# Kernel tuning notes

Measured on AMD Instinct MI355X. Metric: run time of the kernel, lower is better.

## Reference

```python
import jax, jax.numpy as jnp
import numpy as np

ITERS = 10   # self.iters
REG = 0.1    # self.reg
EPS = 1e-12  # F.normalize eps


def setup_inputs() -> dict:
    key = jax.random.key(0)
    k1, k2 = jax.random.split(key)
    b, n_s, h = 64, 512, 1024
    x = jax.random.normal(k1, (b, n_s, h), dtype=jnp.float32)
    y = jax.random.normal(k2, (b, n_s, h), dtype=jnp.float32)
    return {"x": x, "y": y}


def _l2_normalize(t):
    n = jnp.sqrt(jnp.sum(t * t, axis=-1, keepdims=True))
    return t / jnp.maximum(n, EPS)


def reference(x, y):
    # CosineScorer.score(x, y, get_diag=False) with temperature=1
    xn = _l2_normalize(x)
    yn = _l2_normalize(y)
    scores = jnp.einsum('bmh,bnh->bmn', xn, yn)  # (b, n_s, n_s)
    b, m, n = scores.shape

    # uniform log marginals: -log(n_s)
    log_mu = jnp.full((b, m), -jnp.log(jnp.float32(m)), dtype=scores.dtype)
    log_nu = jnp.full((b, n), -jnp.log(jnp.float32(n)), dtype=scores.dtype)

    # log_ipot: iterative proximal point OT in log space
    A = scores / jnp.float32(REG)

    def step(carry, _):
        v, T = carry
        Q = A + T                                              # (b, m, n)
        u = log_mu - jax.nn.logsumexp(Q + v[:, None, :], axis=2)
        v_new = log_nu - jax.nn.logsumexp(Q + u[:, :, None], axis=1)
        T_new = Q + u[:, :, None] + v_new[:, None, :]
        return (v_new, T_new), None

    init = (log_nu, jnp.zeros_like(scores))
    (_, T), _ = jax.lax.scan(step, init, None, length=ITERS)

    matching = jnp.exp(T)
    return jnp.sum(scores * matching, axis=(1, 2))  # (b,)
```

## Files before the change

### kernel.cpp

```cpp
#include <hip/hip_runtime.h>
#include <hip/hip_fp16.h>

#define NB 64
#define NS 512
#define NH 1024
#define NITERS 10

#define LOG_INV_NS (-6.238324625039508f)

using half8 = _Float16 __attribute__((ext_vector_type(8)));
using f32x4 = float __attribute__((ext_vector_type(4)));

__global__ __launch_bounds__(512) void gemm_fused(
    const float* __restrict__ x, const float* __restrict__ y,
    _Float16* __restrict__ Sh) {
  __shared__ _Float16 As[2][256][72];
  __shared__ _Float16 Bs[2][256][72];
  __shared__ float invA[256], invB[256];

  int blk = blockIdx.x;
  int b = blk & 63;
  int tile = blk >> 6;
  int tm = (tile >> 1) * 256, tn = (tile & 1) * 256;
  int tid = threadIdx.x;
  int wid = tid >> 6, lane = tid & 63;
  int wr = (wid >> 2) * 128;
  int wc = (wid & 3) * 64;
  int fr = lane & 15, fq = lane >> 4;

  int srow = tid >> 1;
  int skh = (tid & 1) * 16;
  const float* xb = x + ((size_t)b * NS + tm + srow) * NH + skh;
  const float* yb = y + ((size_t)b * NS + tn + srow) * NH + skh;

  f32x4 acc[8][4] = {};
  float4 rx[4], ry[4];
  float sqx = 0.f, sqy = 0.f;

#define GLOAD(K0)                                                     \
  do {                                                                \
    const float4* px = (const float4*)(xb + (K0));                    \
    const float4* py = (const float4*)(yb + (K0));                    \
    rx[0] = px[0]; rx[1] = px[1]; rx[2] = px[2]; rx[3] = px[3];       \
    ry[0] = py[0]; ry[1] = py[1]; ry[2] = py[2]; ry[3] = py[3];       \
  } while (0)

#define CAST_WRITE(BUF, COL)                                          \
  do {                                                                \
    alignas(16) _Float16 ta[16];                                      \
    alignas(16) _Float16 tb[16];                                      \
    _Pragma("unroll") for (int j = 0; j < 4; ++j) {                   \
      float4 v = rx[j];                                               \
      ta[4 * j + 0] = (_Float16)v.x; ta[4 * j + 1] = (_Float16)v.y;   \
      ta[4 * j + 2] = (_Float16)v.z; ta[4 * j + 3] = (_Float16)v.w;   \
      sqx += v.x * v.x + v.y * v.y + v.z * v.z + v.w * v.w;           \
    }                                                                 \
    _Pragma("unroll") for (int j = 0; j < 4; ++j) {                   \
      float4 v = ry[j];                                               \
      tb[4 * j + 0] = (_Float16)v.x; tb[4 * j + 1] = (_Float16)v.y;   \
      tb[4 * j + 2] = (_Float16)v.z; tb[4 * j + 3] = (_Float16)v.w;   \
      sqy += v.x * v.x + v.y * v.y + v.z * v.z + v.w * v.w;           \
    }                                                                 \
    *(half8*)&As[BUF][srow][(COL) + skh + 0] = *(half8*)&ta[0];       \
    *(half8*)&As[BUF][srow][(COL) + skh + 8] = *(half8*)&ta[8];       \
    *(half8*)&Bs[BUF][srow][(COL) + skh + 0] = *(half8*)&tb[0];       \
    *(half8*)&Bs[BUF][srow][(COL) + skh + 8] = *(half8*)&tb[8];       \
  } while (0)

  GLOAD(0);
  CAST_WRITE(0, 0);
  GLOAD(32);
  CAST_WRITE(0, 32);
  GLOAD(64);
  asm volatile("s_waitcnt lgkmcnt(0)" ::: "memory");
  __builtin_amdgcn_sched_barrier(0);
  __builtin_amdgcn_s_barrier();
  __builtin_amdgcn_sched_barrier(0);

  for (int s = 0; s < 16; ++s) {
    int cur = s & 1;
    {
      half8 bf[4];
#pragma unroll
      for (int j = 0; j < 4; ++j)
        bf[j] = *(const half8*)&Bs[cur][wc + 16 * j + fr][8 * fq];
#pragma unroll
      for (int i = 0; i < 8; ++i) {
        half8 af = *(const half8*)&As[cur][wr + 16 * i + fr][8 * fq];
#pragma unroll
        for (int j = 0; j < 4; ++j)
          acc[i][j] = __builtin_amdgcn_mfma_f32_16x16x32_f16(af, bf[j], acc[i][j], 0, 0, 0);
      }
    }
    if (s < 15) {
      CAST_WRITE(cur ^ 1, 0);
      GLOAD((s + 1) * 64 + 32);
    }
    {
      half8 bf[4];
#pragma unroll
      for (int j = 0; j < 4; ++j)
        bf[j] = *(const half8*)&Bs[cur][wc + 16 * j + fr][32 + 8 * fq];
#pragma unroll
      for (int i = 0; i < 8; ++i) {
        half8 af = *(const half8*)&As[cur][wr + 16 * i + fr][32 + 8 * fq];
#pragma unroll
        for (int j = 0; j < 4; ++j)
          acc[i][j] = __builtin_amdgcn_mfma_f32_16x16x32_f16(af, bf[j], acc[i][j], 0, 0, 0);
      }
    }
    if (s < 15) {
      CAST_WRITE(cur ^ 1, 32);
      if (s < 14) GLOAD((s + 2) * 64);
    }
    asm volatile("s_waitcnt lgkmcnt(0)" ::: "memory");
    __builtin_amdgcn_sched_barrier(0);
    __builtin_amdgcn_s_barrier();
    __builtin_amdgcn_sched_barrier(0);
  }
#undef GLOAD
#undef CAST_WRITE

  sqx += __shfl_xor(sqx, 1, 64);
  sqy += __shfl_xor(sqy, 1, 64);
  if ((tid & 1) == 0) {
    invA[srow] = 1.0f / fmaxf(sqrtf(sqx), 1e-12f);
    invB[srow] = 1.0f / fmaxf(sqrtf(sqy), 1e-12f);
  }
  __syncthreads();

  _Float16* Sb = Sh + (size_t)b * NS * NS;
#pragma unroll
  for (int i = 0; i < 8; ++i)
#pragma unroll
    for (int j = 0; j < 4; ++j) {
      int rr = wr + 16 * i + 4 * fq;
      int cc = wc + 16 * j + fr;
      float ib = invB[cc];
#pragma unroll
      for (int p = 0; p < 4; ++p)
        Sb[(size_t)(tm + rr + p) * NS + tn + cc] =
            (_Float16)(acc[i][j][p] * invA[rr + p] * ib);
    }
}

__global__ __launch_bounds__(256) void u_kernel(
    const _Float16* __restrict__ Sh, const float* __restrict__ W,
    float* __restrict__ U, float f, int first) {
  __shared__ float Wt[8][65];
  int blk = blockIdx.x;
  int bs = blk & 7, rest = blk >> 3;
  int rowgrp = rest & 31, bq = rest >> 5;
  int b = bq * 8 + bs;
  int t = threadIdx.x;
  if (!first) {
#pragma unroll
    for (int i = 0; i < 2; ++i) {
      int idx = t + 256 * i;
      Wt[idx & 7][idx >> 3] = W[b * NS + idx];
    }
    __syncthreads();
  }
  int w = t >> 6, l = t & 63;
  float wn[8];
#pragma unroll
  for (int e = 0; e < 8; ++e) wn[e] = first ? LOG_INV_NS : Wt[e][l];
  int m0 = rowgrp * 16 + w * 4;
  const _Float16* Sb = Sh + ((size_t)b * NS + m0) * NS + 8 * l;
  float sum[4] = {0.f, 0.f, 0.f, 0.f};
#pragma unroll
  for (int k = 0; k < 4; ++k) {
    half8 hv = *(const half8*)(Sb + (size_t)k * NS);
#pragma unroll
    for (int e = 0; e < 8; ++e) sum[k] += __expf(fmaf(f, (float)hv[e], wn[e]));
  }
#pragma unroll
  for (int o = 32; o; o >>= 1) {
#pragma unroll
    for (int k = 0; k < 4; ++k) sum[k] += __shfl_xor(sum[k], o, 64);
  }
  if (l == 0) {
#pragma unroll
    for (int k = 0; k < 4; ++k)
      U[b * NS + m0 + k] = LOG_INV_NS - __logf(sum[k]);
  }
}

__global__ __launch_bounds__(256) void v_kernel(
    const _Float16* __restrict__ Sh, const float* __restrict__ U,
    float* __restrict__ V, float* __restrict__ W,
    float f, int first, int last, float* __restrict__ outPart) {
  __shared__ float Ul[NS];
  __shared__ float partC[64][33];
  __shared__ float partD[64][33];
  __shared__ float redC[4][33];
  __shared__ float redD[4][33];
  int blk = blockIdx.x;
  int b = blk & 63;
  int ng = blk >> 6;
  int t = threadIdx.x;
  Ul[t] = U[b * NS + t];
  Ul[t + 256] = U[b * NS + t + 256];
  __syncthreads();

  int oct = t & 3;
  int mc = t >> 2;
  const _Float16* Sb = Sh + (size_t)b * NS * NS + (size_t)(mc * 8) * NS + ng * 32 + oct * 8;
  float c[8] = {}, d[8] = {};
#pragma unroll
  for (int i = 0; i < 8; ++i) {
    half8 hv = *(const half8*)(Sb + (size_t)i * NS);
    float um = Ul[mc * 8 + i];
#pragma unroll
    for (int e = 0; e < 8; ++e) {
      float sv = (float)hv[e];
      float ev = __expf(fmaf(f, sv, um));
      c[e] += ev;
      d[e] = fmaf(sv, ev, d[e]);
    }
  }
#pragma unroll
  for (int e = 0; e < 8; ++e) {
    partC[mc][oct * 8 + e] = c[e];
    partD[mc][oct * 8 + e] = d[e];
  }
  __syncthreads();
  {
    int ci = t & 31, seg = t >> 5;
    float cc = 0.f, dd = 0.f;
#pragma unroll
    for (int k = 0; k < 8; ++k) {
      cc += partC[seg * 8 + k][ci];
      dd += partD[seg * 8 + k][ci];
    }
    cc += __shfl_xor(cc, 32, 64);
    dd += __shfl_xor(dd, 32, 64);
    int w = t >> 6, l = t & 63;
    if (l < 32) { redC[w][l] = cc; redD[w][l] = dd; }
  }
  __syncthreads();
  if (t < 32) {
    float cc = redC[0][t] + redC[1][t] + redC[2][t] + redC[3][t];
    float vnew = LOG_INV_NS - __logf(cc);
    int n = b * NS + ng * 32 + t;
    float vold = first ? 0.f : V[n];
    V[n] = vnew;
    W[n] = 2.f * vnew - vold;
    if (last) {
      float dd = redD[0][t] + redD[1][t] + redD[2][t] + redD[3][t];
      float r = dd / cc;
      r += __shfl_xor(r, 16, 64);
      r += __shfl_xor(r, 8, 64);
      r += __shfl_xor(r, 4, 64);
      r += __shfl_xor(r, 2, 64);
      r += __shfl_xor(r, 1, 64);
      if (t == 0) outPart[b * 16 + ng] = r * (1.0f / (float)NS);
    }
  }
}

__global__ void combine_kernel(const float* __restrict__ outPart, float* __restrict__ out) {
  int b = threadIdx.x;
  float s = 0.f;
#pragma unroll
  for (int k = 0; k < 16; ++k) s += outPart[b * 16 + k];
  out[b] = s;
}

extern "C" void kernel_launch(void* const* d_in, const int* in_sizes, int n_in,
                              void* d_out, int out_size, void* d_ws, size_t ws_size,
                              hipStream_t stream) {
  (void)in_sizes; (void)n_in; (void)out_size; (void)ws_size;
  const float* x = (const float*)d_in[0];
  const float* y = (const float*)d_in[1];
  float* out = (float*)d_out;

  char* ws = (char*)d_ws;
  _Float16* Sh = (_Float16*)ws;
  float* fregion = (float*)(ws + (size_t)NB * NS * NS * 2);
  float* U = fregion;
  float* V = U + NB * NS;
  float* W = V + NB * NS;
  float* outPart = W + NB * NS;

  gemm_fused<<<256, 512, 0, stream>>>(x, y, Sh);

  for (int t = 1; t <= NITERS; ++t) {
    float f = 10.0f * (float)t;
    u_kernel<<<2048, 256, 0, stream>>>(Sh, W, U, f, t == 1 ? 1 : 0);
    v_kernel<<<1024, 256, 0, stream>>>(Sh, U, V, W, f, t == 1 ? 1 : 0,
                                       t == NITERS ? 1 : 0, outPart);
  }
  combine_kernel<<<1, 64, 0, stream>>>(outPart, out);
}
```

Measured before the change: 192.8 us.

## Stage fp32 tiles via direct global-to-LDS loads with XOR swizzle

```diff
diff --git a/kernel.cpp b/kernel.cpp
--- a/kernel.cpp
+++ b/kernel.cpp
@@ -11,11 +11,16 @@
 using half8 = _Float16 __attribute__((ext_vector_type(8)));
 using f32x4 = float __attribute__((ext_vector_type(4)));
 
+#define GLOAD_LDS(G, L)                                                  \
+  __builtin_amdgcn_global_load_lds(                                      \
+      (const __attribute__((address_space(1))) unsigned int*)(G),        \
+      (__attribute__((address_space(3))) unsigned int*)(L), 16, 0, 0)
+
 __global__ __launch_bounds__(512) void gemm_fused(
     const float* __restrict__ x, const float* __restrict__ y,
     _Float16* __restrict__ Sh) {
-  __shared__ _Float16 As[2][256][72];
-  __shared__ _Float16 Bs[2][256][72];
+  __shared__ float As32[2][8192];
+  __shared__ float Bs32[2][8192];
   __shared__ float invA[256], invB[256];
 
   int blk = blockIdx.x;
@@ -28,104 +33,103 @@
   int wc = (wid & 3) * 64;
   int fr = lane & 15, fq = lane >> 4;
 
-  int srow = tid >> 1;
-  int skh = (tid & 1) * 16;
-  const float* xb = x + ((size_t)b * NS + tm + srow) * NH + skh;
-  const float* yb = y + ((size_t)b * NS + tn + srow) * NH + skh;
+  int rql = wid * 32 + (lane >> 3);
+  int colf = 4 * ((lane & 7) ^ (rql & 7));
+  const float* xg0 = x + ((size_t)(b * NS + tm + rql)) * NH + colf;
+  const float* yg0 = y + ((size_t)(b * NS + tn + rql)) * NH + colf;
 
   f32x4 acc[8][4] = {};
-  float4 rx[4], ry[4];
-  float sqx = 0.f, sqy = 0.f;
-
-#define GLOAD(K0)                                                     \
-  do {                                                                \
-    const float4* px = (const float4*)(xb + (K0));                    \
-    const float4* py = (const float4*)(yb + (K0));                    \
-    rx[0] = px[0]; rx[1] = px[1]; rx[2] = px[2]; rx[3] = px[3];       \
-    ry[0] = py[0]; ry[1] = py[1]; ry[2] = py[2]; ry[3] = py[3];       \
+  float pa[4] = {0.f, 0.f, 0.f, 0.f};
+  float pb[4] = {0.f, 0.f, 0.f, 0.f};
+
+#define GSTAGE(CH, BUF)                                                  \
+  do {                                                                   \
+    int k0g = (CH) * 32;                                                 \
+    _Pragma("unroll") for (int q = 0; q < 4; ++q) {                      \
+      GLOAD_LDS(xg0 + (size_t)(q * 8) * NH + k0g,                        \
+                &As32[BUF][wid * 1024 + q * 256]);                       \
+      GLOAD_LDS(yg0 + (size_t)(q * 8) * NH + k0g,                        \
+                &Bs32[BUF][wid * 1024 + q * 256]);                       \
+    }                                                                    \
   } while (0)
 
-#define CAST_WRITE(BUF, COL)                                          \
-  do {                                                                \
-    alignas(16) _Float16 ta[16];                                      \
-    alignas(16) _Float16 tb[16];                                      \
-    _Pragma("unroll") for (int j = 0; j < 4; ++j) {                   \
-      float4 v = rx[j];                                               \
-      ta[4 * j + 0] = (_Float16)v.x; ta[4 * j + 1] = (_Float16)v.y;   \
-      ta[4 * j + 2] = (_Float16)v.z; ta[4 * j + 3] = (_Float16)v.w;   \
-      sqx += v.x * v.x + v.y * v.y + v.z * v.z + v.w * v.w;           \
-    }                                                                 \
-    _Pragma("unroll") for (int j = 0; j < 4; ++j) {                   \
-      float4 v = ry[j];                                               \
-      tb[4 * j + 0] = (_Float16)v.x; tb[4 * j + 1] = (_Float16)v.y;   \
-      tb[4 * j + 2] = (_Float16)v.z; tb[4 * j + 3] = (_Float16)v.w;   \
-      sqy += v.x * v.x + v.y * v.y + v.z * v.z + v.w * v.w;           \
-    }                                                                 \
-    *(half8*)&As[BUF][srow][(COL) + skh + 0] = *(half8*)&ta[0];       \
-    *(half8*)&As[BUF][srow][(COL) + skh + 8] = *(half8*)&ta[8];       \
-    *(half8*)&Bs[BUF][srow][(COL) + skh + 0] = *(half8*)&tb[0];       \
-    *(half8*)&Bs[BUF][srow][(COL) + skh + 8] = *(half8*)&tb[8];       \
-  } while (0)
-
-  GLOAD(0);
-  CAST_WRITE(0, 0);
-  GLOAD(32);
-  CAST_WRITE(0, 32);
-  GLOAD(64);
-  asm volatile("s_waitcnt lgkmcnt(0)" ::: "memory");
+  GSTAGE(0, 0);
+  GSTAGE(1, 1);
+  asm volatile("s_waitcnt vmcnt(8)" ::: "memory");
   __builtin_amdgcn_sched_barrier(0);
   __builtin_amdgcn_s_barrier();
   __builtin_amdgcn_sched_barrier(0);
 
-  for (int s = 0; s < 16; ++s) {
+  for (int s = 0; s < 32; ++s) {
     int cur = s & 1;
+    const char* bA = (const char*)&As32[cur][0];
+    const char* bB = (const char*)&Bs32[cur][0];
+
+    half8 bf[4];
+#pragma unroll
+    for (int j = 0; j < 4; ++j) {
+      int R = wc + 16 * j + fr;
+      unsigned p0 = (unsigned)(R * 128 + fq * 32);
+      unsigned sw = (unsigned)((R & 7) << 4);
+      float4 b0 = *(const float4*)(bB + (p0 ^ sw));
+      float4 b1 = *(const float4*)(bB + ((p0 + 16) ^ sw));
+      bf[j] = half8{(_Float16)b0.x, (_Float16)b0.y, (_Float16)b0.z, (_Float16)b0.w,
+                    (_Float16)b1.x, (_Float16)b1.y, (_Float16)b1.z, (_Float16)b1.w};
+    }
+#pragma unroll
+    for (int i = 0; i < 8; ++i) {
+      int R = wr + 16 * i + fr;
+      unsigned p0 = (unsigned)(R * 128 + fq * 32);
+      unsigned sw = (unsigned)((R & 7) << 4);
+      float4 a0 = *(const float4*)(bA + (p0 ^ sw));
+      float4 a1 = *(const float4*)(bA + ((p0 + 16) ^ sw));
+      half8 af = half8{(_Float16)a0.x, (_Float16)a0.y, (_Float16)a0.z, (_Float16)a0.w,
+                       (_Float16)a1.x, (_Float16)a1.y, (_Float16)a1.z, (_Float16)a1.w};
+#pragma unroll
+      for (int j = 0; j < 4; ++j)
+        acc[i][j] = __builtin_amdgcn_mfma_f32_16x16x32_f16(af, bf[j], acc[i][j], 0, 0, 0);
+    }
     {
-      half8 bf[4];
-#pragma unroll
-      for (int j = 0; j < 4; ++j)
-        bf[j] = *(const half8*)&Bs[cur][wc + 16 * j + fr][8 * fq];
-#pragma unroll
-      for (int i = 0; i < 8; ++i) {
-        half8 af = *(const half8*)&As[cur][wr + 16 * i + fr][8 * fq];
-#pragma unroll
-        for (int j = 0; j < 4; ++j)
-          acc[i][j] = __builtin_amdgcn_mfma_f32_16x16x32_f16(af, bf[j], acc[i][j], 0, 0, 0);
+      const float4* nA = (const float4*)&As32[cur][wid * 1024];
+      const float4* nB = (const float4*)&Bs32[cur][wid * 1024];
+#pragma unroll
+      for (int q = 0; q < 4; ++q) {
+        float4 va = nA[q * 64 + lane];
+        float4 vb = nB[q * 64 + lane];
+        pa[q] += va.x * va.x + va.y * va.y + va.z * va.z + va.w * va.w;
+        pb[q] += vb.x * vb.x + vb.y * vb.y + vb.z * vb.z + vb.w * vb.w;
       }
     }
-    if (s < 15) {
-      CAST_WRITE(cur ^ 1, 0);
-      GLOAD((s + 1) * 64 + 32);
-    }
-    {
-      half8 bf[4];
-#pragma unroll
-      for (int j = 0; j < 4; ++j)
-        bf[j] = *(const half8*)&Bs[cur][wc + 16 * j + fr][32 + 8 * fq];
-#pragma unroll
-      for (int i = 0; i < 8; ++i) {
-        half8 af = *(const half8*)&As[cur][wr + 16 * i + fr][32 + 8 * fq];
-#pragma unroll
-        for (int j = 0; j < 4; ++j)
-          acc[i][j] = __builtin_amdgcn_mfma_f32_16x16x32_f16(af, bf[j], acc[i][j], 0, 0, 0);
-      }
-    }
-    if (s < 15) {
-      CAST_WRITE(cur ^ 1, 32);
-      if (s < 14) GLOAD((s + 2) * 64);
-    }
     asm volatile("s_waitcnt lgkmcnt(0)" ::: "memory");
     __builtin_amdgcn_sched_barrier(0);
     __builtin_amdgcn_s_barrier();
     __builtin_amdgcn_sched_barrier(0);
-  }
-#undef GLOAD
-#undef CAST_WRITE
-
-  sqx += __shfl_xor(sqx, 1, 64);
-  sqy += __shfl_xor(sqy, 1, 64);
-  if ((tid & 1) == 0) {
-    invA[srow] = 1.0f / fmaxf(sqrtf(sqx), 1e-12f);
-    invB[srow] = 1.0f / fmaxf(sqrtf(sqy), 1e-12f);
+    if (s < 30) GSTAGE(s + 2, cur);
+    if (s < 30)
+      asm volatile("s_waitcnt vmcnt(8)" ::: "memory");
+    else
+      asm volatile("s_waitcnt vmcnt(0)" ::: "memory");
+    __builtin_amdgcn_sched_barrier(0);
+    __builtin_amdgcn_s_barrier();
+    __builtin_amdgcn_sched_barrier(0);
+  }
+#undef GSTAGE
+
+#pragma unroll
+  for (int q = 0; q < 4; ++q) {
+#pragma unroll
+    for (int mask = 1; mask <= 4; mask <<= 1) {
+      pa[q] += __shfl_xor(pa[q], mask, 64);
+      pb[q] += __shfl_xor(pb[q], mask, 64);
+    }
+  }
+  if ((lane & 7) == 0) {
+    int rbase = wid * 32 + (lane >> 3);
+#pragma unroll
+    for (int q = 0; q < 4; ++q) {
+      invA[rbase + q * 8] = 1.0f / fmaxf(sqrtf(pa[q]), 1e-12f);
+      invB[rbase + q * 8] = 1.0f / fmaxf(sqrtf(pb[q]), 1e-12f);
+    }
   }
   __syncthreads();
 
```

New measurement: 215.9 us. 12.0% more time.

## Fuse row and column logsumexp passes into one kernel per iteration

Applied to the files above, without the earlier changes.

```diff
diff --git a/kernel.cpp b/kernel.cpp
--- a/kernel.cpp
+++ b/kernel.cpp
@@ -144,27 +144,14 @@
     }
 }
 
-__global__ __launch_bounds__(256) void u_kernel(
-    const _Float16* __restrict__ Sh, const float* __restrict__ W,
-    float* __restrict__ U, float f, int first) {
-  __shared__ float Wt[8][65];
+__global__ __launch_bounds__(256) void u_first_kernel(
+    const _Float16* __restrict__ Sh, float* __restrict__ U, float f) {
   int blk = blockIdx.x;
   int bs = blk & 7, rest = blk >> 3;
   int rowgrp = rest & 31, bq = rest >> 5;
   int b = bq * 8 + bs;
   int t = threadIdx.x;
-  if (!first) {
-#pragma unroll
-    for (int i = 0; i < 2; ++i) {
-      int idx = t + 256 * i;
-      Wt[idx & 7][idx >> 3] = W[b * NS + idx];
-    }
-    __syncthreads();
-  }
   int w = t >> 6, l = t & 63;
-  float wn[8];
-#pragma unroll
-  for (int e = 0; e < 8; ++e) wn[e] = first ? LOG_INV_NS : Wt[e][l];
   int m0 = rowgrp * 16 + w * 4;
   const _Float16* Sb = Sh + ((size_t)b * NS + m0) * NS + 8 * l;
   float sum[4] = {0.f, 0.f, 0.f, 0.f};
@@ -172,7 +159,7 @@
   for (int k = 0; k < 4; ++k) {
     half8 hv = *(const half8*)(Sb + (size_t)k * NS);
 #pragma unroll
-    for (int e = 0; e < 8; ++e) sum[k] += __expf(fmaf(f, (float)hv[e], wn[e]));
+    for (int e = 0; e < 8; ++e) sum[k] += __expf(fmaf(f, (float)hv[e], LOG_INV_NS));
   }
 #pragma unroll
   for (int o = 32; o; o >>= 1) {
@@ -186,43 +173,73 @@
   }
 }
 
-__global__ __launch_bounds__(256) void v_kernel(
-    const _Float16* __restrict__ Sh, const float* __restrict__ U,
-    float* __restrict__ V, float* __restrict__ W,
-    float f, int first, int last, float* __restrict__ outPart) {
+__global__ __launch_bounds__(256) void p_kernel(
+    const _Float16* __restrict__ Sh, const float* __restrict__ Ufirst,
+    float* __restrict__ V, float* __restrict__ rowpart,
+    float f, float fnext, int first, int last, float* __restrict__ outPart) {
   __shared__ float Ul[NS];
   __shared__ float partC[64][33];
   __shared__ float partD[64][33];
   __shared__ float redC[4][33];
   __shared__ float redD[4][33];
+  __shared__ float Wl[32];
+  __shared__ float partR[NS][5];
+
   int blk = blockIdx.x;
   int b = blk & 63;
   int ng = blk >> 6;
   int t = threadIdx.x;
-  Ul[t] = U[b * NS + t];
-  Ul[t + 256] = U[b * NS + t + 256];
+  int w = t >> 6, l = t & 63;
+
+  if (first) {
+    Ul[t] = Ufirst[b * NS + t];
+    Ul[t + 256] = Ufirst[b * NS + t + 256];
+  } else {
+    const float* rp = rowpart + (size_t)b * 16 * NS;
+    float s0 = 0.f, s1 = 0.f;
+#pragma unroll
+    for (int k = 0; k < 16; ++k) {
+      s0 += rp[k * NS + t];
+      s1 += rp[k * NS + t + 256];
+    }
+    Ul[t] = LOG_INV_NS - __logf(s0);
+    Ul[t + 256] = LOG_INV_NS - __logf(s1);
+  }
   __syncthreads();
 
   int oct = t & 3;
   int mc = t >> 2;
-  const _Float16* Sb = Sh + (size_t)b * NS * NS + (size_t)(mc * 8) * NS + ng * 32 + oct * 8;
+  const _Float16* Sbc = Sh + (size_t)b * NS * NS + (size_t)(mc * 8) * NS + ng * 32 + oct * 8;
+  half8 hv[8];
+#pragma unroll
+  for (int i = 0; i < 8; ++i) hv[i] = *(const half8*)(Sbc + (size_t)i * NS);
+
   float c[8] = {}, d[8] = {};
-#pragma unroll
-  for (int i = 0; i < 8; ++i) {
-    half8 hv = *(const half8*)(Sb + (size_t)i * NS);
-    float um = Ul[mc * 8 + i];
-#pragma unroll
-    for (int e = 0; e < 8; ++e) {
-      float sv = (float)hv[e];
-      float ev = __expf(fmaf(f, sv, um));
-      c[e] += ev;
-      d[e] = fmaf(sv, ev, d[e]);
+  if (!last) {
+#pragma unroll
+    for (int i = 0; i < 8; ++i) {
+      float um = Ul[mc * 8 + i];
+#pragma unroll
+      for (int e = 0; e < 8; ++e)
+        c[e] += __expf(fmaf(f, (float)hv[i][e], um));
+    }
+  } else {
+#pragma unroll
+    for (int i = 0; i < 8; ++i) {
+      float um = Ul[mc * 8 + i];
+#pragma unroll
+      for (int e = 0; e < 8; ++e) {
+        float sv = (float)hv[i][e];
+        float ev = __expf(fmaf(f, sv, um));
+        c[e] += ev;
+        d[e] = fmaf(sv, ev, d[e]);
+      }
     }
   }
 #pragma unroll
   for (int e = 0; e < 8; ++e) {
     partC[mc][oct * 8 + e] = c[e];
-    partD[mc][oct * 8 + e] = d[e];
+    if (last) partD[mc][oct * 8 + e] = d[e];
   }
   __syncthreads();
   {
@@ -231,22 +248,22 @@
 #pragma unroll
     for (int k = 0; k < 8; ++k) {
       cc += partC[seg * 8 + k][ci];
-      dd += partD[seg * 8 + k][ci];
+      if (last) dd += partD[seg * 8 + k][ci];
     }
     cc += __shfl_xor(cc, 32, 64);
-    dd += __shfl_xor(dd, 32, 64);
-    int w = t >> 6, l = t & 63;
-    if (l < 32) { redC[w][l] = cc; redD[w][l] = dd; }
+    if (last) dd += __shfl_xor(dd, 32, 64);
+    if (l < 32) { redC[w][l] = cc; if (last) redD[w][l] = dd; }
   }
   __syncthreads();
   if (t < 32) {
     float cc = redC[0][t] + redC[1][t] + redC[2][t] + redC[3][t];
-    float vnew = LOG_INV_NS - __logf(cc);
-    int n = b * NS + ng * 32 + t;
-    float vold = first ? 0.f : V[n];
-    V[n] = vnew;
-    W[n] = 2.f * vnew - vold;
-    if (last) {
+    if (!last) {
+      float vnew = LOG_INV_NS - __logf(cc);
+      int n = b * NS + ng * 32 + t;
+      float vold = first ? 0.f : V[n];
+      V[n] = vnew;
+      Wl[t] = 2.f * vnew - vold;
+    } else {
       float dd = redD[0][t] + redD[1][t] + redD[2][t] + redD[3][t];
       float r = dd / cc;
       r += __shfl_xor(r, 16, 64);
@@ -257,6 +274,28 @@
       if (t == 0) outPart[b * 16 + ng] = r * (1.0f / (float)NS);
     }
   }
+  if (last) return;
+  __syncthreads();
+
+  float wl[8];
+#pragma unroll
+  for (int e = 0; e < 8; ++e) wl[e] = Wl[oct * 8 + e];
+#pragma unroll
+  for (int i = 0; i < 8; ++i) {
+    float s = 0.f;
+#pragma unroll
+    for (int e = 0; e < 8; ++e)
+      s += __expf(fmaf(fnext, (float)hv[i][e], wl[e]));
+    partR[mc * 8 + i][oct] = s;
+  }
+  __syncthreads();
+  {
+    float* rp = rowpart + ((size_t)b * 16 + ng) * NS;
+    float q0 = partR[t][0] + partR[t][1] + partR[t][2] + partR[t][3];
+    float q1 = partR[t + 256][0] + partR[t + 256][1] + partR[t + 256][2] + partR[t + 256][3];
+    rp[t] = q0;
+    rp[t + 256] = q1;
+  }
 }
 
 __global__ void combine_kernel(const float* __restrict__ outPart, float* __restrict__ out) {
@@ -280,16 +319,17 @@
   float* fregion = (float*)(ws + (size_t)NB * NS * NS * 2);
   float* U = fregion;
   float* V = U + NB * NS;
-  float* W = V + NB * NS;
-  float* outPart = W + NB * NS;
+  float* outPart = V + NB * NS;
+  float* rowpart = outPart + 1024;
 
   gemm_fused<<<256, 512, 0, stream>>>(x, y, Sh);
+  u_first_kernel<<<2048, 256, 0, stream>>>(Sh, U, 10.0f);
 
   for (int t = 1; t <= NITERS; ++t) {
-    float f = 10.0f * (float)t;
-    u_kernel<<<2048, 256, 0, stream>>>(Sh, W, U, f, t == 1 ? 1 : 0);
-    v_kernel<<<1024, 256, 0, stream>>>(Sh, U, V, W, f, t == 1 ? 1 : 0,
-                                       t == NITERS ? 1 : 0, outPart);
+    p_kernel<<<1024, 256, 0, stream>>>(Sh, U, V, rowpart,
+                                       10.0f * (float)t, 10.0f * (float)(t + 1),
+                                       t == 1 ? 1 : 0, t == NITERS ? 1 : 0,
+                                       outPart);
   }
   combine_kernel<<<1, 64, 0, stream>>>(outPart, out);
 }
```

New measurement: 178.7 us. 1.08x faster.
